# Optimization experiments

Hardware: AMD Instinct MI355X
Metric: run time of the kernel (lower is better)

## Reference

```python
import jax, jax.numpy as jnp
import numpy as np

B, L, HID = 32, 1, 3072
H, KV, D = 16, 8, 256
S = 2048
SCALE = D ** -0.5


def setup_inputs() -> dict:
    key = jax.random.key(0)
    ks = jax.random.split(key, 10)
    return {
        "hidden_states": jax.random.normal(ks[0], (B, L, HID), jnp.float32),
        "freqs_cos": jax.random.normal(ks[1], (B, L, D // 2), jnp.float32),
        "freqs_sin": jax.random.normal(ks[2], (B, L, D // 2), jnp.float32),
        "mask": jnp.zeros((B, 1, 1, S), jnp.float32),
        "cache_k": jax.random.normal(ks[3], (B, KV, S, D), jnp.float32),
        "cache_v": jax.random.normal(ks[4], (B, KV, S, D), jnp.float32),
        "wq": jax.random.normal(ks[5], (HID, H * D), jnp.float32) * 0.02,
        "wk": jax.random.normal(ks[6], (HID, KV * D), jnp.float32) * 0.02,
        "wv": jax.random.normal(ks[7], (HID, KV * D), jnp.float32) * 0.02,
        "wo": jax.random.normal(ks[8], (H * D, HID), jnp.float32) * 0.02,
        "pos": 2047,
    }


def _rope(x, cos, sin):
    # x: [B, L, nh, D]; cos/sin: [B, L, D/2]. Split-half complex rotation:
    # pairs are (x[..., i], x[..., i + D/2]), matching torch chunk+view_as_complex.
    half = x.shape[-1] // 2
    xr, xi = x[..., :half], x[..., half:]
    c = cos[:, :, None, :]
    s = sin[:, :, None, :]
    return jnp.concatenate([xr * c - xi * s, xr * s + xi * c], axis=-1)


def reference(hidden_states, freqs_cos, freqs_sin, mask, cache_k, cache_v,
              wq, wk, wv, wo, pos):
    G = H // KV  # queries per kv head
    xq = (hidden_states @ wq).reshape(B, L, H, D)
    xk = (hidden_states @ wk).reshape(B, L, KV, D)
    xv = (hidden_states @ wv).reshape(B, L, KV, D)

    xq = _rope(xq, freqs_cos, freqs_sin)
    xk = _rope(xk, freqs_cos, freqs_sin)

    # [B, heads, L, D]
    xq = xq.transpose(0, 2, 1, 3)
    xk = xk.transpose(0, 2, 1, 3)
    xv = xv.transpose(0, 2, 1, 3)

    # insert current step into the KV cache at static position `pos`
    cache_k = cache_k.at[:, :, pos:pos + L, :].set(xk)
    cache_v = cache_v.at[:, :, pos:pos + L, :].set(xv)

    # GQA attention over the full cache without materializing repeated KV
    q = xq.reshape(B, KV, G, L, D)
    scores = jnp.einsum('bkgqd,bksd->bkgqs', q, cache_k) * SCALE
    scores = scores + mask[:, :, None]  # [B,1,1,1,S] broadcast
    probs = jax.nn.softmax(scores, axis=-1)
    out = jnp.einsum('bkgqs,bksd->bkgqd', probs, cache_v)

    out = out.reshape(B, H, L, D).transpose(0, 2, 1, 3).reshape(B, L, H * D)
    return out @ wo
```

## Files before the change

kernel.cpp:

```cpp
#include <hip/hip_runtime.h>
#include <hip/hip_bf16.h>


#define SCALE_ 0.0625f

#define NKC   24u
#define OFF_XQKV (NKC*32u*8192u)
#define OFF_PO   (OFF_XQKV + 262144u)
#define OFF_ML   (1048576u)

typedef float f32x4 __attribute__((ext_vector_type(4)));

__device__ inline f32x4 ntl4(const float* p) {
  return __builtin_nontemporal_load((const f32x4*)p);
}
__device__ inline void nts4(float* p, f32x4 v) {
  __builtin_nontemporal_store(v, (f32x4*)p);
}
__device__ inline f32x4 ld4(const float* p) { return *(const f32x4*)p; }

__device__ inline void fma4(float4& a, float s, const float4& w) {
  a.x = fmaf(s, w.x, a.x); a.y = fmaf(s, w.y, a.y);
  a.z = fmaf(s, w.z, a.z); a.w = fmaf(s, w.w, a.w);
}
__device__ inline float dot4v(f32x4 a, f32x4 b) {
  return a.x * b.x + a.y * b.y + a.z * b.z + a.w * b.w;
}

__global__ __launch_bounds__(256) void qkv_partial_kernel(
    const float* __restrict__ x, const float* __restrict__ wq,
    const float* __restrict__ wk, const float* __restrict__ wv,
    float* __restrict__ pqkv) {
  __shared__ float xls[32][128];

  const int lane = threadIdx.x & 63;
  const int bg   = threadIdx.x >> 6;
  const int ctile = blockIdx.x & 31;
  const int kc    = blockIdx.x >> 5;
  const int n = ctile * 256 + lane * 4;

  for (int i = threadIdx.x; i < 1024; i += 256) {
    const int b = i >> 5;
    const int r = i & 31;
    *(f32x4*)(&xls[b][r * 4]) = ld4(x + (size_t)b * 3072 + kc * 128 + r * 4);
  }

  const float* w; int stride, nn;
  if (n < 4096)      { w = wq; stride = 4096; nn = n; }
  else if (n < 6144) { w = wk; stride = 2048; nn = n - 4096; }
  else               { w = wv; stride = 2048; nn = n - 6144; }
  const float* wb = w + (size_t)(kc * 128) * stride + nn;

  f32x4 acc[8];
#pragma unroll
  for (int j = 0; j < 8; ++j) acc[j] = (f32x4){0.f, 0.f, 0.f, 0.f};

  __syncthreads();

  f32x4 wA[4], wB[4];
#define LDW(S, KK)                                                   \
  {                                                                  \
    S[0] = ntl4(wb + (size_t)((KK) + 0) * stride);                   \
    S[1] = ntl4(wb + (size_t)((KK) + 1) * stride);                   \
    S[2] = ntl4(wb + (size_t)((KK) + 2) * stride);                   \
    S[3] = ntl4(wb + (size_t)((KK) + 3) * stride);                   \
  }
#define CMP(S, KK)                                                   \
  {                                                                  \
    _Pragma("unroll")                                                \
    for (int j = 0; j < 8; ++j) {                                    \
      const f32x4 xv = *(const f32x4*)(&xls[bg * 8 + j][(KK)]);      \
      acc[j] += xv.x * S[0];                                         \
      acc[j] += xv.y * S[1];                                         \
      acc[j] += xv.z * S[2];                                         \
      acc[j] += xv.w * S[3];                                         \
    }                                                                \
  }

  LDW(wA, 0);
  for (int k = 0; k < 128; k += 8) {
    LDW(wB, k + 4);
    CMP(wA, k);
    const int kn = (k + 8 < 128) ? (k + 8) : 0;
    LDW(wA, kn);
    CMP(wB, k + 4);
  }
#undef LDW
#undef CMP

#pragma unroll
  for (int j = 0; j < 8; ++j) {
    nts4(pqkv + ((size_t)kc * 32 + bg * 8 + j) * 8192 + n, acc[j]);
  }
}

__global__ __launch_bounds__(256) void reduce_rope_kernel(
    const float* __restrict__ pqkv, const float* __restrict__ fcos,
    const float* __restrict__ fsin, float* __restrict__ xqkv) {
  const int w = blockIdx.x * 256 + threadIdx.x;
  const int b = w / 1280;
  const int r = w - b * 1280;
  const float* pb = pqkv + (size_t)b * 8192;
  float* ob = xqkv + (size_t)b * 8192;

  if (r < 768) {
    int n1, d;
    const bool isq = (r < 512);
    if (isq) { const int h = r >> 5; d = (r & 31) * 4; n1 = h * 256 + d; }
    else     { const int p = r - 512; const int kvh = p >> 5; d = (p & 31) * 4;
               n1 = 4096 + kvh * 256 + d; }
    const int n2 = n1 + 128;
    f32x4 xr = (f32x4){0.f, 0.f, 0.f, 0.f};
    f32x4 xi = (f32x4){0.f, 0.f, 0.f, 0.f};
    for (int kc = 0; kc < (int)NKC; ++kc) {
      xr += ntl4(pb + (size_t)kc * 262144 + n1);
      xi += ntl4(pb + (size_t)kc * 262144 + n2);
    }
    const f32x4 c = ld4(fcos + b * 128 + d);
    const f32x4 s = ld4(fsin + b * 128 + d);
    f32x4 o1 = xr * c - xi * s;
    f32x4 o2 = xr * s + xi * c;
    if (isq) { o1 *= SCALE_; o2 *= SCALE_; }
    *(f32x4*)(ob + n1) = o1;
    *(f32x4*)(ob + n2) = o2;
  } else {
    const int nn = 6144 + (r - 768) * 4;
    f32x4 v = (f32x4){0.f, 0.f, 0.f, 0.f};
    for (int kc = 0; kc < (int)NKC; ++kc) {
      v += ntl4(pb + (size_t)kc * 262144 + nn);
    }
    *(f32x4*)(ob + nn) = v;
  }
}

__global__ __launch_bounds__(256) void attn_chunk_kernel(
    const float* __restrict__ xqkv, const float* __restrict__ cache_k,
    const float* __restrict__ cache_v, const float* __restrict__ mask,
    const int* __restrict__ posp, float* __restrict__ opart,
    float* __restrict__ ml) {
  __shared__ float accbuf[8][512];
  __shared__ float mred[8][4];

  const int tid = threadIdx.x, lane = tid & 63, wv = tid >> 6;
  const int sub = lane & 31;
  const int stream = wv * 2 + (lane >> 5);
  const int c  = blockIdx.x & 7;
  const int kv = (blockIdx.x >> 3) & 7;
  const int b  = blockIdx.x >> 6;
  const int pos = posp[0];
  const int s0 = c * 256;
  const int dbase = sub * 8;

  const float* xb = xqkv + (size_t)b * 8192;
  const float* knew = xb + 4096 + kv * 256;
  const float* vnew = xb + 6144 + kv * 256;
  const size_t base = ((size_t)b * 8 + kv) * 2048 * 256;
  const float* kbase = cache_k + base;
  const float* vbase = cache_v + base;
  const float* mrow = mask + (size_t)b * 2048;

  const f32x4 qa0 = ld4(xb + (kv * 2 + 0) * 256 + dbase);
  const f32x4 qa1 = ld4(xb + (kv * 2 + 0) * 256 + dbase + 4);
  const f32x4 qb0 = ld4(xb + (kv * 2 + 1) * 256 + dbase);
  const f32x4 qb1 = ld4(xb + (kv * 2 + 1) * 256 + dbase + 4);

  float m0 = -3.4e38f, l0 = 0.f, m1 = -3.4e38f, l1 = 0.f;
  f32x4 a00 = (f32x4){0.f, 0.f, 0.f, 0.f};
  f32x4 a01 = (f32x4){0.f, 0.f, 0.f, 0.f};
  f32x4 a10 = (f32x4){0.f, 0.f, 0.f, 0.f};
  f32x4 a11 = (f32x4){0.f, 0.f, 0.f, 0.f};

  int sA = s0 + stream;
  int sB = sA + 8;
  const float* krA = (sA == pos) ? knew : (kbase + (size_t)sA * 256);
  const float* vrA = (sA == pos) ? vnew : (vbase + (size_t)sA * 256);
  const float* krB = (sB == pos) ? knew : (kbase + (size_t)sB * 256);
  const float* vrB = (sB == pos) ? vnew : (vbase + (size_t)sB * 256);
  f32x4 kA0 = ntl4(krA + dbase);
  f32x4 kA1 = ntl4(krA + dbase + 4);
  f32x4 vA0 = ntl4(vrA + dbase);
  f32x4 vA1 = ntl4(vrA + dbase + 4);
  float mkA = mrow[sA];
  f32x4 kB0 = ntl4(krB + dbase);
  f32x4 kB1 = ntl4(krB + dbase + 4);
  f32x4 vB0 = ntl4(vrB + dbase);
  f32x4 vB1 = ntl4(vrB + dbase + 4);
  float mkB = mrow[sB];

  for (int i = 0; i < 32; i += 2) {
    {
      float d0 = dot4v(qa0, kA0) + dot4v(qa1, kA1);
      float d1 = dot4v(qb0, kA0) + dot4v(qb1, kA1);
      const int ipf = (i + 2 < 32) ? (i + 2) : 31;
      const int sn = s0 + stream + 8 * ipf;
      const float* krn = (sn == pos) ? knew : (kbase + (size_t)sn * 256);
      const float* vrn = (sn == pos) ? vnew : (vbase + (size_t)sn * 256);
      kA0 = ntl4(krn + dbase);
      kA1 = ntl4(krn + dbase + 4);
      const float mkn = mrow[sn];
#pragma unroll
      for (int off = 16; off > 0; off >>= 1) {
        d0 += __shfl_xor(d0, off);
        d1 += __shfl_xor(d1, off);
      }
      d0 += mkA; d1 += mkA;
      const float nm0 = fmaxf(m0, d0);
      const float al0 = __expf(m0 - nm0);
      const float p0  = __expf(d0 - nm0);
      m0 = nm0; l0 = fmaf(l0, al0, p0);
      a00 = a00 * al0 + p0 * vA0;
      a01 = a01 * al0 + p0 * vA1;
      const float nm1 = fmaxf(m1, d1);
      const float al1 = __expf(m1 - nm1);
      const float p1  = __expf(d1 - nm1);
      m1 = nm1; l1 = fmaf(l1, al1, p1);
      a10 = a10 * al1 + p1 * vA0;
      a11 = a11 * al1 + p1 * vA1;
      vA0 = ntl4(vrn + dbase);
      vA1 = ntl4(vrn + dbase + 4);
      mkA = mkn;
    }
    {
      float d0 = dot4v(qa0, kB0) + dot4v(qa1, kB1);
      float d1 = dot4v(qb0, kB0) + dot4v(qb1, kB1);
      const int ipf = (i + 3 < 32) ? (i + 3) : 31;
      const int sn = s0 + stream + 8 * ipf;
      const float* krn = (sn == pos) ? knew : (kbase + (size_t)sn * 256);
      const float* vrn = (sn == pos) ? vnew : (vbase + (size_t)sn * 256);
      kB0 = ntl4(krn + dbase);
      kB1 = ntl4(krn + dbase + 4);
      const float mkn = mrow[sn];
#pragma unroll
      for (int off = 16; off > 0; off >>= 1) {
        d0 += __shfl_xor(d0, off);
        d1 += __shfl_xor(d1, off);
      }
      d0 += mkB; d1 += mkB;
      const float nm0 = fmaxf(m0, d0);
      const float al0 = __expf(m0 - nm0);
      const float p0  = __expf(d0 - nm0);
      m0 = nm0; l0 = fmaf(l0, al0, p0);
      a00 = a00 * al0 + p0 * vB0;
      a01 = a01 * al0 + p0 * vB1;
      const float nm1 = fmaxf(m1, d1);
      const float al1 = __expf(m1 - nm1);
      const float p1  = __expf(d1 - nm1);
      m1 = nm1; l1 = fmaf(l1, al1, p1);
      a10 = a10 * al1 + p1 * vB0;
      a11 = a11 * al1 + p1 * vB1;
      vB0 = ntl4(vrn + dbase);
      vB1 = ntl4(vrn + dbase + 4);
      mkB = mkn;
    }
  }

  if (sub == 0) {
    mred[stream][0] = m0; mred[stream][1] = l0;
    mred[stream][2] = m1; mred[stream][3] = l1;
  }
  __syncthreads();
  float M0 = -3.4e38f, M1 = -3.4e38f;
#pragma unroll
  for (int t = 0; t < 8; ++t) {
    M0 = fmaxf(M0, mred[t][0]);
    M1 = fmaxf(M1, mred[t][2]);
  }
  const float sc0 = __expf(m0 - M0);
  const float sc1 = __expf(m1 - M1);
  float* ab = &accbuf[stream][0];
  ab[dbase + 0] = a00.x * sc0; ab[dbase + 1] = a00.y * sc0;
  ab[dbase + 2] = a00.z * sc0; ab[dbase + 3] = a00.w * sc0;
  ab[dbase + 4] = a01.x * sc0; ab[dbase + 5] = a01.y * sc0;
  ab[dbase + 6] = a01.z * sc0; ab[dbase + 7] = a01.w * sc0;
  ab[256 + dbase + 0] = a10.x * sc1; ab[256 + dbase + 1] = a10.y * sc1;
  ab[256 + dbase + 2] = a10.z * sc1; ab[256 + dbase + 3] = a10.w * sc1;
  ab[256 + dbase + 4] = a11.x * sc1; ab[256 + dbase + 5] = a11.y * sc1;
  ab[256 + dbase + 6] = a11.z * sc1; ab[256 + dbase + 7] = a11.w * sc1;
  __syncthreads();

  if (tid == 0) {
    float L0 = 0.f, L1 = 0.f;
#pragma unroll
    for (int t = 0; t < 8; ++t) {
      L0 = fmaf(mred[t][1], __expf(mred[t][0] - M0), L0);
      L1 = fmaf(mred[t][3], __expf(mred[t][2] - M1), L1);
    }
    float2* mlp = (float2*)ml;
    const int mlbase = (((b * 8 + kv) * 8) + c) * 2;
    mlp[mlbase + 0] = make_float2(M0, L0);
    mlp[mlbase + 1] = make_float2(M1, L1);
  }

  const size_t obase = (size_t)((b * 8 + kv) * 8 + c) * 512;
  for (int t = tid; t < 512; t += 256) {
    float sum = 0.f;
#pragma unroll
    for (int st = 0; st < 8; ++st) sum += accbuf[st][t];
    opart[obase + t] = sum;
  }
}

__global__ __launch_bounds__(256) void oproj_fused_kernel(
    const float* __restrict__ opart, const float* __restrict__ ml,
    const float* __restrict__ wo, float* __restrict__ po) {
  __shared__ float xs[32][128];

  const int t = threadIdx.x;
  const int ctile = blockIdx.x % 24;
  const int rem   = blockIdx.x / 24;
  const int kc    = rem >> 1;
  const int kh    = rem & 1;
  const int kvh = kc >> 1, g = kc & 1;

  {
    const int b = t >> 3;
    const int dloc = (t & 7) * 16;
    const int kvb = b * 8 + kvh;
    const float2* mlp = (const float2*)ml;
    float2 mls[8];
    float M = -3.4e38f;
#pragma unroll
    for (int c = 0; c < 8; ++c) {
      mls[c] = mlp[(kvb * 8 + c) * 2 + g];
      M = fmaxf(M, mls[c].x);
    }
    float L = 0.f;
    f32x4 O[4];
#pragma unroll
    for (int q = 0; q < 4; ++q) O[q] = (f32x4){0.f, 0.f, 0.f, 0.f};
#pragma unroll
    for (int c = 0; c < 8; ++c) {
      const float wc = __expf(mls[c].x - M);
      L = fmaf(mls[c].y, wc, L);
      const float* src = opart +
          (size_t)(kvb * 8 + c) * 512 + g * 256 + kh * 128 + dloc;
#pragma unroll
      for (int q = 0; q < 4; ++q) O[q] += wc * ld4(src + q * 4);
    }
    const float invL = 1.f / L;
#pragma unroll
    for (int q = 0; q < 4; ++q) {
      *(f32x4*)(&xs[b][dloc + q * 4]) = O[q] * invL;
    }
  }
  __syncthreads();

  const int lane = t & 31;
  const int half = t >> 5;
  const int n = ctile * 128 + lane * 4;
  const float* wb = wo + (size_t)(kc * 256 + kh * 128) * 3072 + n;

  f32x4 acc[4];
#pragma unroll
  for (int j = 0; j < 4; ++j) acc[j] = (f32x4){0.f, 0.f, 0.f, 0.f};

  f32x4 wA[4], wB[4];
#define LDW(S, KK)                                                 \
  {                                                                \
    S[0] = ntl4(wb + (size_t)((KK) + 0) * 3072);                   \
    S[1] = ntl4(wb + (size_t)((KK) + 1) * 3072);                   \
    S[2] = ntl4(wb + (size_t)((KK) + 2) * 3072);                   \
    S[3] = ntl4(wb + (size_t)((KK) + 3) * 3072);                   \
  }
#define CMP(S, KK)                                                 \
  {                                                                \
    _Pragma("unroll")                                              \
    for (int j = 0; j < 4; ++j) {                                  \
      const f32x4 xv = *(const f32x4*)(&xs[half * 4 + j][(KK)]);   \
      acc[j] += xv.x * S[0];                                       \
      acc[j] += xv.y * S[1];                                       \
      acc[j] += xv.z * S[2];                                       \
      acc[j] += xv.w * S[3];                                       \
    }                                                              \
  }

  LDW(wA, 0);
  for (int k = 0; k < 128; k += 8) {
    LDW(wB, k + 4);
    CMP(wA, k);
    const int kn = (k + 8 < 128) ? (k + 8) : 0;
    LDW(wA, kn);
    CMP(wB, k + 4);
  }
#undef LDW
#undef CMP

#pragma unroll
  for (int j = 0; j < 4; ++j) {
    *(f32x4*)(po + ((size_t)(kc * 2 + kh) * 32 + half * 4 + j) * 3072 + n)
        = acc[j];
  }
}

__global__ __launch_bounds__(256) void finalize_kernel(
    const float* __restrict__ po, float* __restrict__ out) {
  const int i = blockIdx.x * 256 + threadIdx.x;
  f32x4 acc = (f32x4){0.f, 0.f, 0.f, 0.f};
#pragma unroll
  for (int kc = 0; kc < 32; ++kc) {
    acc += ntl4(po + ((size_t)kc * 24576 + i) * 4);
  }
  *(f32x4*)((float*)out + (size_t)i * 4) = acc;
}

extern "C" void kernel_launch(void* const* d_in, const int* in_sizes, int n_in,
                              void* d_out, int out_size, void* d_ws, size_t ws_size,
                              hipStream_t stream) {
  (void)in_sizes; (void)n_in; (void)out_size; (void)ws_size;
  const float* x    = (const float*)d_in[0];
  const float* fcos = (const float*)d_in[1];
  const float* fsin = (const float*)d_in[2];
  const float* mask = (const float*)d_in[3];
  const float* ck   = (const float*)d_in[4];
  const float* cv   = (const float*)d_in[5];
  const float* wq   = (const float*)d_in[6];
  const float* wk   = (const float*)d_in[7];
  const float* wv   = (const float*)d_in[8];
  const float* wo   = (const float*)d_in[9];
  const int*   pos  = (const int*)d_in[10];

  float* ws    = (float*)d_ws;
  float* pqkv  = ws;
  float* opart = ws;
  float* ml    = ws + OFF_ML;
  float* xqkv  = ws + OFF_XQKV;
  float* po    = ws + OFF_PO;
  float* out   = (float*)d_out;

  qkv_partial_kernel<<<768, 256, 0, stream>>>(x, wq, wk, wv, pqkv);
  reduce_rope_kernel<<<160, 256, 0, stream>>>(pqkv, fcos, fsin, xqkv);
  attn_chunk_kernel<<<2048, 256, 0, stream>>>(xqkv, ck, cv, mask, pos, opart, ml);
  oproj_fused_kernel<<<768, 256, 0, stream>>>(opart, ml, wo, po);
  finalize_kernel<<<96, 256, 0, stream>>>(po, out);
}
```

Baseline: 304.8 us.

## Fuse QKV reduction and RoPE into attention kernel, widen QKV projection blocks

Removes the separate reduce/RoPE kernel: each attention block now sums the 24 K-chunk partials for its own q/k/v slices, applies RoPE and scaling in shared memory, then runs attention. This saves a launch and the intermediate xqkv round trip. The cost is that each (b,kv) slice's partials are re-reduced by all 8 chunk blocks, adding redundant global reads. The QKV partial kernel moves to 512 threads with 4 batch rows per wave, and the grid is reordered chunk-major.

Result: slower. 335.8 us (+10.2%).

```diff
diff --git a/kernel.cpp b/kernel.cpp
--- a/kernel.cpp
+++ b/kernel.cpp
@@ -4,10 +4,10 @@
 
 #define SCALE_ 0.0625f
 
-#define NKC   24u
-#define OFF_XQKV (NKC*32u*8192u)
-#define OFF_PO   (OFF_XQKV + 262144u)
-#define OFF_ML   (1048576u)
+#define NKC       24u
+#define OFF_PO    (NKC*32u*8192u)
+#define OFF_OPART (OFF_PO + 3145728u)
+#define OFF_ML    (OFF_OPART + 1048576u)
 
 typedef float f32x4 __attribute__((ext_vector_type(4)));
 
@@ -19,15 +19,11 @@
 }
 __device__ inline f32x4 ld4(const float* p) { return *(const f32x4*)p; }
 
-__device__ inline void fma4(float4& a, float s, const float4& w) {
-  a.x = fmaf(s, w.x, a.x); a.y = fmaf(s, w.y, a.y);
-  a.z = fmaf(s, w.z, a.z); a.w = fmaf(s, w.w, a.w);
-}
 __device__ inline float dot4v(f32x4 a, f32x4 b) {
   return a.x * b.x + a.y * b.y + a.z * b.z + a.w * b.w;
 }
 
-__global__ __launch_bounds__(256) void qkv_partial_kernel(
+__global__ __launch_bounds__(512) void qkv_partial_kernel(
     const float* __restrict__ x, const float* __restrict__ wq,
     const float* __restrict__ wk, const float* __restrict__ wv,
     float* __restrict__ pqkv) {
@@ -39,7 +35,7 @@
   const int kc    = blockIdx.x >> 5;
   const int n = ctile * 256 + lane * 4;
 
-  for (int i = threadIdx.x; i < 1024; i += 256) {
+  for (int i = threadIdx.x; i < 1024; i += 512) {
     const int b = i >> 5;
     const int r = i & 31;
     *(f32x4*)(&xls[b][r * 4]) = ld4(x + (size_t)b * 3072 + kc * 128 + r * 4);
@@ -51,9 +47,9 @@
   else               { w = wv; stride = 2048; nn = n - 6144; }
   const float* wb = w + (size_t)(kc * 128) * stride + nn;
 
-  f32x4 acc[8];
-#pragma unroll
-  for (int j = 0; j < 8; ++j) acc[j] = (f32x4){0.f, 0.f, 0.f, 0.f};
+  f32x4 acc[4];
+#pragma unroll
+  for (int j = 0; j < 4; ++j) acc[j] = (f32x4){0.f, 0.f, 0.f, 0.f};
 
   __syncthreads();
 
@@ -68,8 +64,8 @@
 #define CMP(S, KK)                                                   \
   {                                                                  \
     _Pragma("unroll")                                                \
-    for (int j = 0; j < 8; ++j) {                                    \
-      const f32x4 xv = *(const f32x4*)(&xls[bg * 8 + j][(KK)]);      \
+    for (int j = 0; j < 4; ++j) {                                    \
+      const f32x4 xv = *(const f32x4*)(&xls[bg * 4 + j][(KK)]);      \
       acc[j] += xv.x * S[0];                                         \
       acc[j] += xv.y * S[1];                                         \
       acc[j] += xv.z * S[2];                                         \
@@ -89,80 +85,96 @@
 #undef CMP
 
 #pragma unroll
-  for (int j = 0; j < 8; ++j) {
-    nts4(pqkv + ((size_t)kc * 32 + bg * 8 + j) * 8192 + n, acc[j]);
-  }
-}
-
-__global__ __launch_bounds__(256) void reduce_rope_kernel(
+  for (int j = 0; j < 4; ++j) {
+    nts4(pqkv + ((size_t)kc * 32 + bg * 4 + j) * 8192 + n, acc[j]);
+  }
+}
+
+__global__ __launch_bounds__(256) void attn_fused_kernel(
     const float* __restrict__ pqkv, const float* __restrict__ fcos,
-    const float* __restrict__ fsin, float* __restrict__ xqkv) {
-  const int w = blockIdx.x * 256 + threadIdx.x;
-  const int b = w / 1280;
-  const int r = w - b * 1280;
-  const float* pb = pqkv + (size_t)b * 8192;
-  float* ob = xqkv + (size_t)b * 8192;
-
-  if (r < 768) {
-    int n1, d;
-    const bool isq = (r < 512);
-    if (isq) { const int h = r >> 5; d = (r & 31) * 4; n1 = h * 256 + d; }
-    else     { const int p = r - 512; const int kvh = p >> 5; d = (p & 31) * 4;
-               n1 = 4096 + kvh * 256 + d; }
-    const int n2 = n1 + 128;
-    f32x4 xr = (f32x4){0.f, 0.f, 0.f, 0.f};
-    f32x4 xi = (f32x4){0.f, 0.f, 0.f, 0.f};
-    for (int kc = 0; kc < (int)NKC; ++kc) {
-      xr += ntl4(pb + (size_t)kc * 262144 + n1);
-      xi += ntl4(pb + (size_t)kc * 262144 + n2);
-    }
-    const f32x4 c = ld4(fcos + b * 128 + d);
-    const f32x4 s = ld4(fsin + b * 128 + d);
-    f32x4 o1 = xr * c - xi * s;
-    f32x4 o2 = xr * s + xi * c;
-    if (isq) { o1 *= SCALE_; o2 *= SCALE_; }
-    *(f32x4*)(ob + n1) = o1;
-    *(f32x4*)(ob + n2) = o2;
-  } else {
-    const int nn = 6144 + (r - 768) * 4;
-    f32x4 v = (f32x4){0.f, 0.f, 0.f, 0.f};
-    for (int kc = 0; kc < (int)NKC; ++kc) {
-      v += ntl4(pb + (size_t)kc * 262144 + nn);
-    }
-    *(f32x4*)(ob + nn) = v;
-  }
-}
-
-__global__ __launch_bounds__(256) void attn_chunk_kernel(
-    const float* __restrict__ xqkv, const float* __restrict__ cache_k,
+    const float* __restrict__ fsin, const float* __restrict__ cache_k,
     const float* __restrict__ cache_v, const float* __restrict__ mask,
     const int* __restrict__ posp, float* __restrict__ opart,
     float* __restrict__ ml) {
-  __shared__ float accbuf[8][512];
+  __shared__ float accraw[8][512];
+  __shared__ float xv[4][256];
   __shared__ float mred[8][4];
 
   const int tid = threadIdx.x, lane = tid & 63, wv = tid >> 6;
   const int sub = lane & 31;
   const int stream = wv * 2 + (lane >> 5);
-  const int c  = blockIdx.x & 7;
-  const int kv = (blockIdx.x >> 3) & 7;
-  const int b  = blockIdx.x >> 6;
+  const int bkv = blockIdx.x & 255;
+  const int c   = blockIdx.x >> 8;
+  const int b  = bkv >> 3;
+  const int kv = bkv & 7;
   const int pos = posp[0];
   const int s0 = c * 256;
   const int dbase = sub * 8;
 
-  const float* xb = xqkv + (size_t)b * 8192;
-  const float* knew = xb + 4096 + kv * 256;
-  const float* vnew = xb + 6144 + kv * 256;
+  {
+    const int sec = tid >> 6;
+    const int idx = (tid & 63) * 4;
+    int nsec;
+    if (sec == 0)      nsec = (kv * 2 + 0) * 256;
+    else if (sec == 1) nsec = (kv * 2 + 1) * 256;
+    else if (sec == 2) nsec = 4096 + kv * 256;
+    else               nsec = 6144 + kv * 256;
+    const float* pb = pqkv + (size_t)b * 8192 + nsec + idx;
+    f32x4 ssum = (f32x4){0.f, 0.f, 0.f, 0.f};
+#pragma unroll
+    for (int kc = 0; kc < (int)NKC; ++kc) {
+      ssum += ld4(pb + (size_t)kc * 262144);
+    }
+    *(f32x4*)(&accraw[0][sec * 256 + idx]) = ssum;
+    __syncthreads();
+    f32x4 outv;
+    const float* raw = &accraw[0][0];
+    if (sec < 3) {
+      if (idx < 128) {
+        const f32x4 xr = ld4(raw + sec * 256 + idx);
+        const f32x4 xi = ld4(raw + sec * 256 + idx + 128);
+        const f32x4 cc = ld4(fcos + b * 128 + idx);
+        const f32x4 ss = ld4(fsin + b * 128 + idx);
+        outv = xr * cc - xi * ss;
+      } else {
+        const int dd = idx - 128;
+        const f32x4 xr = ld4(raw + sec * 256 + dd);
+        const f32x4 xi = ld4(raw + sec * 256 + idx);
+        const f32x4 cc = ld4(fcos + b * 128 + dd);
+        const f32x4 ss = ld4(fsin + b * 128 + dd);
+        outv = xr * ss + xi * cc;
+      }
+      if (sec < 2) outv *= SCALE_;
+    } else {
+      outv = ld4(raw + 3 * 256 + idx);
+    }
+    __syncthreads();
+    *(f32x4*)(&xv[sec][idx]) = outv;
+    __syncthreads();
+  }
+
   const size_t base = ((size_t)b * 8 + kv) * 2048 * 256;
   const float* kbase = cache_k + base;
   const float* vbase = cache_v + base;
   const float* mrow = mask + (size_t)b * 2048;
 
-  const f32x4 qa0 = ld4(xb + (kv * 2 + 0) * 256 + dbase);
-  const f32x4 qa1 = ld4(xb + (kv * 2 + 0) * 256 + dbase + 4);
-  const f32x4 qb0 = ld4(xb + (kv * 2 + 1) * 256 + dbase);
-  const f32x4 qb1 = ld4(xb + (kv * 2 + 1) * 256 + dbase + 4);
+  const f32x4 qa0 = ld4(&xv[0][dbase]);
+  const f32x4 qa1 = ld4(&xv[0][dbase + 4]);
+  const f32x4 qb0 = ld4(&xv[1][dbase]);
+  const f32x4 qb1 = ld4(&xv[1][dbase + 4]);
+  const f32x4 kn0 = ld4(&xv[2][dbase]);
+  const f32x4 kn1 = ld4(&xv[2][dbase + 4]);
+  const f32x4 vn0 = ld4(&xv[3][dbase]);
+  const f32x4 vn1 = ld4(&xv[3][dbase + 4]);
+
+#define LDK(K0, K1, S)                                          \
+  { const float* kr_ = kbase + (size_t)(S) * 256;               \
+    K0 = ntl4(kr_ + dbase); K1 = ntl4(kr_ + dbase + 4);         \
+    if ((S) == pos) { K0 = kn0; K1 = kn1; } }
+#define LDV(V0, V1, S)                                          \
+  { const float* vr_ = vbase + (size_t)(S) * 256;               \
+    V0 = ntl4(vr_ + dbase); V1 = ntl4(vr_ + dbase + 4);         \
+    if ((S) == pos) { V0 = vn0; V1 = vn1; } }
 
   float m0 = -3.4e38f, l0 = 0.f, m1 = -3.4e38f, l1 = 0.f;
   f32x4 a00 = (f32x4){0.f, 0.f, 0.f, 0.f};
@@ -170,21 +182,12 @@
   f32x4 a10 = (f32x4){0.f, 0.f, 0.f, 0.f};
   f32x4 a11 = (f32x4){0.f, 0.f, 0.f, 0.f};
 
-  int sA = s0 + stream;
-  int sB = sA + 8;
-  const float* krA = (sA == pos) ? knew : (kbase + (size_t)sA * 256);
-  const float* vrA = (sA == pos) ? vnew : (vbase + (size_t)sA * 256);
-  const float* krB = (sB == pos) ? knew : (kbase + (size_t)sB * 256);
-  const float* vrB = (sB == pos) ? vnew : (vbase + (size_t)sB * 256);
-  f32x4 kA0 = ntl4(krA + dbase);
-  f32x4 kA1 = ntl4(krA + dbase + 4);
-  f32x4 vA0 = ntl4(vrA + dbase);
-  f32x4 vA1 = ntl4(vrA + dbase + 4);
+  const int sA = s0 + stream;
+  const int sB = sA + 8;
+  f32x4 kA0, kA1, vA0, vA1, kB0, kB1, vB0, vB1;
+  LDK(kA0, kA1, sA); LDV(vA0, vA1, sA);
   float mkA = mrow[sA];
-  f32x4 kB0 = ntl4(krB + dbase);
-  f32x4 kB1 = ntl4(krB + dbase + 4);
-  f32x4 vB0 = ntl4(vrB + dbase);
-  f32x4 vB1 = ntl4(vrB + dbase + 4);
+  LDK(kB0, kB1, sB); LDV(vB0, vB1, sB);
   float mkB = mrow[sB];
 
   for (int i = 0; i < 32; i += 2) {
@@ -193,10 +196,7 @@
       float d1 = dot4v(qb0, kA0) + dot4v(qb1, kA1);
       const int ipf = (i + 2 < 32) ? (i + 2) : 31;
       const int sn = s0 + stream + 8 * ipf;
-      const float* krn = (sn == pos) ? knew : (kbase + (size_t)sn * 256);
-      const float* vrn = (sn == pos) ? vnew : (vbase + (size_t)sn * 256);
-      kA0 = ntl4(krn + dbase);
-      kA1 = ntl4(krn + dbase + 4);
+      LDK(kA0, kA1, sn);
       const float mkn = mrow[sn];
 #pragma unroll
       for (int off = 16; off > 0; off >>= 1) {
@@ -216,8 +216,7 @@
       m1 = nm1; l1 = fmaf(l1, al1, p1);
       a10 = a10 * al1 + p1 * vA0;
       a11 = a11 * al1 + p1 * vA1;
-      vA0 = ntl4(vrn + dbase);
-      vA1 = ntl4(vrn + dbase + 4);
+      LDV(vA0, vA1, sn);
       mkA = mkn;
     }
     {
@@ -225,10 +224,7 @@
       float d1 = dot4v(qb0, kB0) + dot4v(qb1, kB1);
       const int ipf = (i + 3 < 32) ? (i + 3) : 31;
       const int sn = s0 + stream + 8 * ipf;
-      const float* krn = (sn == pos) ? knew : (kbase + (size_t)sn * 256);
-      const float* vrn = (sn == pos) ? vnew : (vbase + (size_t)sn * 256);
-      kB0 = ntl4(krn + dbase);
-      kB1 = ntl4(krn + dbase + 4);
+      LDK(kB0, kB1, sn);
       const float mkn = mrow[sn];
 #pragma unroll
       for (int off = 16; off > 0; off >>= 1) {
@@ -248,11 +244,12 @@
       m1 = nm1; l1 = fmaf(l1, al1, p1);
       a10 = a10 * al1 + p1 * vB0;
       a11 = a11 * al1 + p1 * vB1;
-      vB0 = ntl4(vrn + dbase);
-      vB1 = ntl4(vrn + dbase + 4);
+      LDV(vB0, vB1, sn);
       mkB = mkn;
     }
   }
+#undef LDK
+#undef LDV
 
   if (sub == 0) {
     mred[stream][0] = m0; mred[stream][1] = l0;
@@ -267,7 +264,7 @@
   }
   const float sc0 = __expf(m0 - M0);
   const float sc1 = __expf(m1 - M1);
-  float* ab = &accbuf[stream][0];
+  float* ab = &accraw[stream][0];
   ab[dbase + 0] = a00.x * sc0; ab[dbase + 1] = a00.y * sc0;
   ab[dbase + 2] = a00.z * sc0; ab[dbase + 3] = a00.w * sc0;
   ab[dbase + 4] = a01.x * sc0; ab[dbase + 5] = a01.y * sc0;
@@ -286,16 +283,16 @@
       L1 = fmaf(mred[t][3], __expf(mred[t][2] - M1), L1);
     }
     float2* mlp = (float2*)ml;
-    const int mlbase = (((b * 8 + kv) * 8) + c) * 2;
+    const int mlbase = ((bkv * 8) + c) * 2;
     mlp[mlbase + 0] = make_float2(M0, L0);
     mlp[mlbase + 1] = make_float2(M1, L1);
   }
 
-  const size_t obase = (size_t)((b * 8 + kv) * 8 + c) * 512;
+  const size_t obase = (size_t)(bkv * 8 + c) * 512;
   for (int t = tid; t < 512; t += 256) {
     float sum = 0.f;
 #pragma unroll
-    for (int st = 0; st < 8; ++st) sum += accbuf[st][t];
+    for (int st = 0; st < 8; ++st) sum += accraw[st][t];
     opart[obase + t] = sum;
   }
 }
@@ -421,15 +418,14 @@
 
   float* ws    = (float*)d_ws;
   float* pqkv  = ws;
-  float* opart = ws;
+  float* po    = ws + OFF_PO;
+  float* opart = ws + OFF_OPART;
   float* ml    = ws + OFF_ML;
-  float* xqkv  = ws + OFF_XQKV;
-  float* po    = ws + OFF_PO;
   float* out   = (float*)d_out;
 
-  qkv_partial_kernel<<<768, 256, 0, stream>>>(x, wq, wk, wv, pqkv);
-  reduce_rope_kernel<<<160, 256, 0, stream>>>(pqkv, fcos, fsin, xqkv);
-  attn_chunk_kernel<<<2048, 256, 0, stream>>>(xqkv, ck, cv, mask, pos, opart, ml);
+  qkv_partial_kernel<<<768, 512, 0, stream>>>(x, wq, wk, wv, pqkv);
+  attn_fused_kernel<<<2048, 256, 0, stream>>>(pqkv, fcos, fsin, ck, cv, mask,
+                                              pos, opart, ml);
   oproj_fused_kernel<<<768, 256, 0, stream>>>(opart, ml, wo, po);
   finalize_kernel<<<96, 256, 0, stream>>>(po, out);
 }
```
